# Kernel tuning notes

Measured on AMD Instinct MI355X. Metric: run time of the kernel, lower is better.

Reference implementation:

```python
import jax, jax.numpy as jnp
import numpy as np

H, W_BINS = 8, 8
EPS = 1e-6
EXTREMA = ((-1.0, 1.0), (-1.0, 1.0))


def setup_inputs() -> dict:
    key = jax.random.key(0)
    k1, k2, k3 = jax.random.split(key, 3)
    B, N, C = 4, 65536, 256
    values = jax.random.normal(k1, (B, N, C), dtype=jnp.float32)
    # coords sampled inside the fixed extrema so the bucketization is in-range
    coords = jax.random.uniform(k2, (N, 2), dtype=jnp.float32, minval=-1.0, maxval=1.0)
    W = jax.random.normal(k3, (H * W_BINS * C, 512), dtype=jnp.float32) * 0.01
    b = jnp.zeros((512,), dtype=jnp.float32)
    return {"values": values, "coords": coords, "W": W, "b": b}


def reference(values, coords, W, b):
    B, N, C = values.shape
    hw = H * W_BINS
    # bin edges, matching torch.linspace(extrema-eps, extrema+eps, steps=h+1)
    Tx = jnp.linspace(EXTREMA[0][0] - EPS, EXTREMA[0][1] + EPS, H + 1)
    Ty = jnp.linspace(EXTREMA[1][0] - EPS, EXTREMA[1][1] + EPS, W_BINS + 1)
    # kx = index of first edge strictly greater than x  (== (Tx <= X).min(-1) argmin)
    kx = jnp.searchsorted(Tx, coords[:, 0], side="right")
    ky = jnp.searchsorted(Ty, coords[:, 1], side="right")
    bins = (kx - 1) + (ky - 1) * H  # [N], in [0, hw)

    # fused segment-mean over all bins in one pass (replaces the per-bin loop)
    vals_nf = values.transpose(1, 0, 2).reshape(N, B * C)  # [N, B*C]
    sums = jax.ops.segment_sum(vals_nf, bins, num_segments=hw)  # [hw, B*C]
    counts = jax.ops.segment_sum(jnp.ones((N,), values.dtype), bins, num_segments=hw)
    means = sums / jnp.maximum(counts, 1.0)[:, None]  # [hw, B*C]
    # cat([ [B,C] for b in range(hw) ], dim=1) -> [B, hw*C]
    out = means.reshape(hw, B, C).transpose(1, 0, 2).reshape(B, hw * C)
    return out @ W + b
```

## Files before the change

### kernel.cpp

```cpp
#include <hip/hip_runtime.h>
#include <cstddef>

#define NPTS   65536
#define BATCH  4
#define CH     256
#define HWBINS 64
#define KDIM   16384
#define JDIM   512
#define CHUNK  32

__device__ __forceinline__ int bucket1d(float xf) {
    const double start = -1.0 - 1e-6;
    const double stop  =  1.0 + 1e-6;
    const double step  = (stop - start) / 8.0;
    double x = (double)xf;
    int k = 0;
#pragma unroll
    for (int i = 0; i < 8; ++i) k += ((double)i * step + start <= x) ? 1 : 0;
    k += (stop <= x) ? 1 : 0;
    int b = k - 1;
    return b < 0 ? 0 : (b > 7 ? 7 : b);
}

__global__ __launch_bounds__(256) void k_zero(float4* __restrict__ sums4,
                                              float4* __restrict__ part4) {
    const int idx = blockIdx.x * 256 + threadIdx.x;
    const float4 z = make_float4(0.f, 0.f, 0.f, 0.f);
    if (idx < 16384) sums4[idx] = z;
    else             part4[idx - 16384] = z;
}

__global__ __launch_bounds__(256) void k_bins(const float* __restrict__ coords,
                                              int* __restrict__ bins,
                                              int* __restrict__ hist_blk) {
    __shared__ int s_h[HWBINS];
    const int tid = threadIdx.x;
    const int blk = blockIdx.x;
    if (tid < HWBINS) s_h[tid] = 0;
    __syncthreads();
#pragma unroll
    for (int i = 0; i < 4; ++i) {
        int n = blk * 1024 + i * 256 + tid;
        float2 xy = *(const float2*)(coords + 2 * (size_t)n);
        int bx = bucket1d(xy.x);
        int by = bucket1d(xy.y);
        int bin = by * 8 + bx;
        bins[n] = bin;
        atomicAdd(&s_h[bin], 1);
    }
    __syncthreads();
    if (tid < HWBINS) hist_blk[blk * HWBINS + tid] = s_h[tid];
}

__global__ void k_scan(const int* __restrict__ hist_blk,
                       int* __restrict__ counts,
                       int* __restrict__ block_base) {
    const int b = threadIdx.x;
    int tot = 0;
#pragma unroll 8
    for (int blk = 0; blk < 64; ++blk) tot += hist_blk[blk * HWBINS + b];
    counts[b] = tot;
    int inc = tot;
#pragma unroll
    for (int d = 1; d < 64; d <<= 1) {
        int v = __shfl_up(inc, d, 64);
        if (b >= d) inc += v;
    }
    int run = inc - tot;
#pragma unroll 8
    for (int blk = 0; blk < 64; ++blk) {
        int h = hist_blk[blk * HWBINS + b];
        block_base[blk * HWBINS + b] = run;
        run += h;
    }
}

__global__ __launch_bounds__(256) void k_scatter(const int* __restrict__ bins,
                                                 const int* __restrict__ block_base,
                                                 int2* __restrict__ pairs) {
    __shared__ int s_cur[HWBINS];
    const int tid = threadIdx.x;
    const int blk = blockIdx.x;
    if (tid < HWBINS) s_cur[tid] = block_base[blk * HWBINS + tid];
    __syncthreads();
#pragma unroll
    for (int i = 0; i < 4; ++i) {
        int n = blk * 1024 + i * 256 + tid;
        int bin = bins[n];
        int pos = atomicAdd(&s_cur[bin], 1);
        pairs[pos] = make_int2(n, bin);
    }
}

__global__ __launch_bounds__(256) void k_seg(const float* __restrict__ values,
                                             const int2* __restrict__ pairs,
                                             float* __restrict__ sums) {
    __shared__ int2 sp[CHUNK];
    const int tid = threadIdx.x;
    const int r0  = blockIdx.x * CHUNK;
    if (tid < CHUNK) sp[tid] = pairs[r0 + tid];
    __syncthreads();

    const int w    = tid >> 6;
    const int lane = tid & 63;
    const float* vb = values + (size_t)w * NPTS * CH + lane * 4;
    float* sb = sums + (size_t)w * HWBINS * CH + lane * 4;

    float4 acc = make_float4(0.f, 0.f, 0.f, 0.f);
    int cur = sp[0].y;

    auto flushfn = [&](int nb) {
        float* d = sb + (size_t)cur * CH;
        unsafeAtomicAdd(d + 0, acc.x);
        unsafeAtomicAdd(d + 1, acc.y);
        unsafeAtomicAdd(d + 2, acc.z);
        unsafeAtomicAdd(d + 3, acc.w);
        acc = make_float4(0.f, 0.f, 0.f, 0.f);
        cur = nb;
    };

    float4 a0 = *(const float4*)(vb + (size_t)sp[0].x * CH);
    float4 a1 = *(const float4*)(vb + (size_t)sp[1].x * CH);
    float4 a2 = *(const float4*)(vb + (size_t)sp[2].x * CH);
    float4 a3 = *(const float4*)(vb + (size_t)sp[3].x * CH);

#pragma unroll
    for (int g = 0; g < CHUNK; g += 4) {
        float4 n0, n1, n2, n3;
        if (g + 4 < CHUNK) {
            n0 = *(const float4*)(vb + (size_t)sp[g + 4].x * CH);
            n1 = *(const float4*)(vb + (size_t)sp[g + 5].x * CH);
            n2 = *(const float4*)(vb + (size_t)sp[g + 6].x * CH);
            n3 = *(const float4*)(vb + (size_t)sp[g + 7].x * CH);
        }
        int b0 = sp[g].y, b1 = sp[g + 1].y, b2 = sp[g + 2].y, b3 = sp[g + 3].y;
        if (b0 != cur) flushfn(b0);
        acc.x += a0.x; acc.y += a0.y; acc.z += a0.z; acc.w += a0.w;
        if (b1 != cur) flushfn(b1);
        acc.x += a1.x; acc.y += a1.y; acc.z += a1.z; acc.w += a1.w;
        if (b2 != cur) flushfn(b2);
        acc.x += a2.x; acc.y += a2.y; acc.z += a2.z; acc.w += a2.w;
        if (b3 != cur) flushfn(b3);
        acc.x += a3.x; acc.y += a3.y; acc.z += a3.z; acc.w += a3.w;
        if (g + 4 < CHUNK) { a0 = n0; a1 = n1; a2 = n2; a3 = n3; }
    }
    flushfn(cur);
}

__global__ __launch_bounds__(256) void k_gemm_a(const float* __restrict__ Wm,
                                                const float* __restrict__ sums,
                                                const int* __restrict__ counts,
                                                float* __restrict__ out_part) {
    __shared__ float s_m[4 * 32];
    const int tid = threadIdx.x;
    const int kc  = blockIdx.x;
    const int k0  = kc * 32;
    if (tid < 128) {
        int bb = tid >> 5, kk = tid & 31, k = k0 + kk;
        float cnt = (float)counts[k >> 8];
        s_m[tid] = sums[(size_t)bb * KDIM + k] / fmaxf(cnt, 1.0f);
    }
    __syncthreads();

    const float2* W2 = (const float2*)Wm;
    const float2* wp = W2 + (size_t)k0 * 256 + tid;
    float2 a0 = {0.f, 0.f}, a1 = {0.f, 0.f}, a2 = {0.f, 0.f}, a3 = {0.f, 0.f};
#pragma unroll
    for (int kk = 0; kk < 32; ++kk) {
        float2 w = wp[(size_t)kk * 256];
        float m0 = s_m[kk], m1 = s_m[32 + kk], m2 = s_m[64 + kk], m3 = s_m[96 + kk];
        a0.x += m0 * w.x; a0.y += m0 * w.y;
        a1.x += m1 * w.x; a1.y += m1 * w.y;
        a2.x += m2 * w.x; a2.y += m2 * w.y;
        a3.x += m3 * w.x; a3.y += m3 * w.y;
    }
    const int slot = kc & 7;
    float* op = out_part + (size_t)slot * 2048 + 2 * tid;
    unsafeAtomicAdd(op + 0,    a0.x); unsafeAtomicAdd(op + 1,    a0.y);
    unsafeAtomicAdd(op + 512,  a1.x); unsafeAtomicAdd(op + 513,  a1.y);
    unsafeAtomicAdd(op + 1024, a2.x); unsafeAtomicAdd(op + 1025, a2.y);
    unsafeAtomicAdd(op + 1536, a3.x); unsafeAtomicAdd(op + 1537, a3.y);
}

__global__ __launch_bounds__(256) void k_gemm_b(const float* __restrict__ out_part,
                                                const float* __restrict__ bias,
                                                float* __restrict__ out) {
    const int idx = blockIdx.x * 256 + threadIdx.x;
    const int j = idx & 511;
    float s = bias[j];
#pragma unroll
    for (int sl = 0; sl < 8; ++sl) s += out_part[(size_t)sl * 2048 + idx];
    out[idx] = s;
}

extern "C" void kernel_launch(void* const* d_in, const int* in_sizes, int n_in,
                              void* d_out, int out_size, void* d_ws, size_t ws_size,
                              hipStream_t stream) {
    const float* values = (const float*)d_in[0];
    const float* coords = (const float*)d_in[1];
    const float* Wm     = (const float*)d_in[2];
    const float* bias   = (const float*)d_in[3];
    float* out = (float*)d_out;

    char* ws = (char*)d_ws;
    int*   bins       = (int*)(ws + 0);
    int*   hist_blk   = (int*)(ws + 262144);
    int*   counts     = (int*)(ws + 278528);
    int*   block_base = (int*)(ws + 278784);
    int2*  pairs      = (int2*)(ws + 295168);
    float* sums       = (float*)(ws + 819456);
    float* out_part   = (float*)(ws + 1081600);

    k_zero   <<<80, 256, 0, stream>>>((float4*)sums, (float4*)out_part);
    k_bins   <<<64, 256, 0, stream>>>(coords, bins, hist_blk);
    k_scan   <<<1, 64, 0, stream>>>(hist_blk, counts, block_base);
    k_scatter<<<64, 256, 0, stream>>>(bins, block_base, pairs);
    k_seg    <<<NPTS / CHUNK, 256, 0, stream>>>(values, pairs, sums);
    k_gemm_a <<<512, 256, 0, stream>>>(Wm, sums, counts, out_part);
    k_gemm_b <<<8, 256, 0, stream>>>(out_part, bias, out);
}
```

Measured before the change: 411.3 us.

## Privatize segment sums across slots, fold zeroing into bins kernel, widen GEMM K-chunk

The segment-sum kernel now accumulates into 8 replicated copies of the sums array, picked by block index, to cut atomic contention on each bin's hot addresses. The GEMM kernel first reduces those copies, takes 64 K rows per block instead of 32, and spreads its partial outputs over 32 slots. The separate zeroing kernel is removed and its work folded into the bins kernel, saving one launch. In exchange the extra slots cost more workspace, more zeroing traffic and extra reads in the reduction stages, and the k_seg chunk size doubles.

After: 396.8 us. 3.5% less time.

```diff
diff --git a/kernel.cpp b/kernel.cpp
--- a/kernel.cpp
+++ b/kernel.cpp
@@ -7,7 +7,9 @@
 #define HWBINS 64
 #define KDIM   16384
 #define JDIM   512
-#define CHUNK  32
+#define CHUNK  64
+#define SSLOTS 8
+#define GSLOTS 32
 
 __device__ __forceinline__ int bucket1d(float xf) {
     const double start = -1.0 - 1e-6;
@@ -22,20 +24,19 @@
     return b < 0 ? 0 : (b > 7 ? 7 : b);
 }
 
-__global__ __launch_bounds__(256) void k_zero(float4* __restrict__ sums4,
-                                              float4* __restrict__ part4) {
-    const int idx = blockIdx.x * 256 + threadIdx.x;
-    const float4 z = make_float4(0.f, 0.f, 0.f, 0.f);
-    if (idx < 16384) sums4[idx] = z;
-    else             part4[idx - 16384] = z;
-}
-
 __global__ __launch_bounds__(256) void k_bins(const float* __restrict__ coords,
                                               int* __restrict__ bins,
-                                              int* __restrict__ hist_blk) {
+                                              int* __restrict__ hist_blk,
+                                              float4* __restrict__ zero4) {
     __shared__ int s_h[HWBINS];
     const int tid = threadIdx.x;
     const int blk = blockIdx.x;
+    {
+        const float4 z = make_float4(0.f, 0.f, 0.f, 0.f);
+        for (int i = blk * 256 + tid; i < (SSLOTS * BATCH * KDIM + GSLOTS * 2048) / 4;
+             i += 64 * 256)
+            zero4[i] = z;
+    }
     if (tid < HWBINS) s_h[tid] = 0;
     __syncthreads();
 #pragma unroll
@@ -94,7 +95,7 @@
 
 __global__ __launch_bounds__(256) void k_seg(const float* __restrict__ values,
                                              const int2* __restrict__ pairs,
-                                             float* __restrict__ sums) {
+                                             float* __restrict__ sums8) {
     __shared__ int2 sp[CHUNK];
     const int tid = threadIdx.x;
     const int r0  = blockIdx.x * CHUNK;
@@ -103,8 +104,9 @@
 
     const int w    = tid >> 6;
     const int lane = tid & 63;
+    const int slot = blockIdx.x & (SSLOTS - 1);
     const float* vb = values + (size_t)w * NPTS * CH + lane * 4;
-    float* sb = sums + (size_t)w * HWBINS * CH + lane * 4;
+    float* sb = sums8 + (size_t)slot * BATCH * KDIM + (size_t)w * KDIM + lane * 4;
 
     float4 acc = make_float4(0.f, 0.f, 0.f, 0.f);
     int cur = sp[0].y;
@@ -148,17 +150,21 @@
 }
 
 __global__ __launch_bounds__(256) void k_gemm_a(const float* __restrict__ Wm,
-                                                const float* __restrict__ sums,
+                                                const float* __restrict__ sums8,
                                                 const int* __restrict__ counts,
                                                 float* __restrict__ out_part) {
-    __shared__ float s_m[4 * 32];
+    __shared__ float s_m[4 * 64];
     const int tid = threadIdx.x;
     const int kc  = blockIdx.x;
-    const int k0  = kc * 32;
-    if (tid < 128) {
-        int bb = tid >> 5, kk = tid & 31, k = k0 + kk;
+    const int k0  = kc * 64;
+    {
+        int bb = tid >> 6, kk = tid & 63, k = k0 + kk;
+        float s = 0.f;
+#pragma unroll
+        for (int sl = 0; sl < SSLOTS; ++sl)
+            s += sums8[(size_t)sl * BATCH * KDIM + (size_t)bb * KDIM + k];
         float cnt = (float)counts[k >> 8];
-        s_m[tid] = sums[(size_t)bb * KDIM + k] / fmaxf(cnt, 1.0f);
+        s_m[tid] = s / fmaxf(cnt, 1.0f);
     }
     __syncthreads();
 
@@ -166,15 +172,15 @@
     const float2* wp = W2 + (size_t)k0 * 256 + tid;
     float2 a0 = {0.f, 0.f}, a1 = {0.f, 0.f}, a2 = {0.f, 0.f}, a3 = {0.f, 0.f};
 #pragma unroll
-    for (int kk = 0; kk < 32; ++kk) {
+    for (int kk = 0; kk < 64; ++kk) {
         float2 w = wp[(size_t)kk * 256];
-        float m0 = s_m[kk], m1 = s_m[32 + kk], m2 = s_m[64 + kk], m3 = s_m[96 + kk];
+        float m0 = s_m[kk], m1 = s_m[64 + kk], m2 = s_m[128 + kk], m3 = s_m[192 + kk];
         a0.x += m0 * w.x; a0.y += m0 * w.y;
         a1.x += m1 * w.x; a1.y += m1 * w.y;
         a2.x += m2 * w.x; a2.y += m2 * w.y;
         a3.x += m3 * w.x; a3.y += m3 * w.y;
     }
-    const int slot = kc & 7;
+    const int slot = kc & (GSLOTS - 1);
     float* op = out_part + (size_t)slot * 2048 + 2 * tid;
     unsafeAtomicAdd(op + 0,    a0.x); unsafeAtomicAdd(op + 1,    a0.y);
     unsafeAtomicAdd(op + 512,  a1.x); unsafeAtomicAdd(op + 513,  a1.y);
@@ -189,7 +195,7 @@
     const int j = idx & 511;
     float s = bias[j];
 #pragma unroll
-    for (int sl = 0; sl < 8; ++sl) s += out_part[(size_t)sl * 2048 + idx];
+    for (int sl = 0; sl < GSLOTS; ++sl) s += out_part[(size_t)sl * 2048 + idx];
     out[idx] = s;
 }
 
@@ -208,14 +214,13 @@
     int*   counts     = (int*)(ws + 278528);
     int*   block_base = (int*)(ws + 278784);
     int2*  pairs      = (int2*)(ws + 295168);
-    float* sums       = (float*)(ws + 819456);
-    float* out_part   = (float*)(ws + 1081600);
-
-    k_zero   <<<80, 256, 0, stream>>>((float4*)sums, (float4*)out_part);
-    k_bins   <<<64, 256, 0, stream>>>(coords, bins, hist_blk);
+    float* sums8      = (float*)(ws + 819456);
+    float* out_part   = (float*)(ws + 2916608);
+
+    k_bins   <<<64, 256, 0, stream>>>(coords, bins, hist_blk, (float4*)sums8);
     k_scan   <<<1, 64, 0, stream>>>(hist_blk, counts, block_base);
     k_scatter<<<64, 256, 0, stream>>>(bins, block_base, pairs);
-    k_seg    <<<NPTS / CHUNK, 256, 0, stream>>>(values, pairs, sums);
-    k_gemm_a <<<512, 256, 0, stream>>>(Wm, sums, counts, out_part);
+    k_seg    <<<NPTS / CHUNK, 256, 0, stream>>>(values, pairs, sums8);
+    k_gemm_a <<<256, 256, 0, stream>>>(Wm, sums8, counts, out_part);
     k_gemm_b <<<8, 256, 0, stream>>>(out_part, bias, out);
 }
```
